# Optimization experiments

Hardware: AMD Instinct MI355X
Metric: run time of the kernel (lower is better)

## Reference

```python
import jax, jax.numpy as jnp
import numpy as np

B, D, NH = 32768, 32, 128
SCALE = 0.05  # weight init scale; keeps exp(s) well-conditioned


def setup_inputs() -> dict:
    key = jax.random.key(0)
    ks = jax.random.split(key, 10)
    x = jax.random.normal(ks[0], (B, D), jnp.float32)
    # layer 0: LeafParam(2) -> learned constant (s, t)
    p0 = jax.random.normal(ks[1], (2,), jnp.float32) * SCALE
    # per-dim MLPs for i = 1..D-1, stacked. Layer i consumes x[:, :i]; we pad
    # its first weight to (D, NH) with rows >= i zeroed so a single batched
    # einsum computes all per-dim nets at once (same math as the python loop).
    mask = (jnp.arange(D)[None, :] < jnp.arange(1, D)[:, None]).astype(jnp.float32)  # (D-1, D)
    W1 = jax.random.normal(ks[2], (D - 1, D, NH), jnp.float32) * SCALE * mask[:, :, None]
    b1 = jax.random.normal(ks[3], (D - 1, NH), jnp.float32) * SCALE
    W2 = jax.random.normal(ks[4], (D - 1, NH, NH), jnp.float32) * SCALE
    b2 = jax.random.normal(ks[5], (D - 1, NH), jnp.float32) * SCALE
    W3 = jax.random.normal(ks[6], (D - 1, NH, NH), jnp.float32) * SCALE
    b3 = jax.random.normal(ks[7], (D - 1, NH), jnp.float32) * SCALE
    W4 = jax.random.normal(ks[8], (D - 1, NH, 2), jnp.float32) * SCALE
    b4 = jax.random.normal(ks[9], (D - 1, 2), jnp.float32) * SCALE
    return dict(x=x, p0=p0, W1=W1, b1=b1, W2=W2, b2=b2, W3=W3, b3=b3, W4=W4, b4=b4)


def _lrelu(h):
    return jnp.where(h >= 0, h, 0.2 * h)  # LeakyReLU(0.2)


def reference(x, p0, W1, b1, W2, b2, W3, b3, W4, b4):
    # All D-1 per-dim MLPs in parallel. W1 rows >= i are zero, so
    h = _lrelu(jnp.einsum('bd,idh->bih', x, W1) + b1[None])     # (B, D-1, NH)
    h = _lrelu(jnp.einsum('bih,ihk->bik', h, W2) + b2[None])
    h = _lrelu(jnp.einsum('bih,ihk->bik', h, W3) + b3[None])
    st = jnp.einsum('bih,iho->bio', h, W4) + b4[None]           # (B, D-1, 2)
    st0 = jnp.broadcast_to(p0[None, None, :], (x.shape[0], 1, 2))
    st = jnp.concatenate([st0, st], axis=1)                     # (B, D, 2)
    s, t = st[..., 0], st[..., 1]
    z = x * jnp.exp(s) + t      # parity=True -> order is the identity permutation
    log_det = jnp.sum(s, axis=1)                                # (B,)
    return z, log_det
```

## Files before the change

kernel.cpp:

```cpp
#include <hip/hip_runtime.h>

typedef __bf16 v8bf  __attribute__((ext_vector_type(8)));
typedef float  f32x4  __attribute__((ext_vector_type(4)));
typedef float  f32x16 __attribute__((ext_vector_type(16)));
typedef unsigned int u32;
typedef u32 u32x4 __attribute__((ext_vector_type(4)));
typedef unsigned short u16;

#define NI   31
#define DD   32
#define NHID 128
#define NROW 32768
#define NCHUNK 64
#define ITERS  2
#define NET_EL 36864
#define W2F_EL 4096
#define W3F_EL 20480
#define LDS_W4T 73728
#define LDS_BB  74240
#define LDS_BYTES 75008

__device__ __forceinline__ u32 cvtpk(float lo, float hi) {
    u32 r;
    asm("v_cvt_pk_bf16_f32 %0, %1, %2" : "=v"(r) : "v"(lo), "v"(hi));
    return r;
}

__device__ __forceinline__ void repack_tile(const f32x16 c, v8bf* f0, v8bf* f1) {
    f32x16 v;
    #pragma unroll
    for (int r = 0; r < 16; ++r) { float x = c[r]; v[r] = fmaxf(x, 0.2f * x); }
    #pragma unroll
    for (int p = 0; p < 2; ++p) {
        u32 a0 = cvtpk(v[8*p + 0], v[8*p + 1]);
        u32 a1 = cvtpk(v[8*p + 2], v[8*p + 3]);
        u32 b0 = cvtpk(v[8*p + 4], v[8*p + 5]);
        u32 b1 = cvtpk(v[8*p + 6], v[8*p + 7]);
        asm("v_permlane32_swap_b32 %0, %1" : "+v"(a0), "+v"(b0));
        asm("v_permlane32_swap_b32 %0, %1" : "+v"(a1), "+v"(b1));
        u32x4 wd = {a0, a1, b0, b1};
        if (p == 0) *f0 = __builtin_bit_cast(v8bf, wd);
        else        *f1 = __builtin_bit_cast(v8bf, wd);
    }
}

__global__ void maf_prep(const float* __restrict__ W1, const float* __restrict__ W2,
                         const float* __restrict__ W3, __bf16* __restrict__ blob,
                         __bf16* __restrict__ xfrag, const float* __restrict__ x) {
    int b = blockIdx.x, t = threadIdx.x;
    if (b < 3 * NI) {
        __shared__ float panel[16 * 128];
        int kind = b / NI, i = b % NI;
        const float* src; __bf16* dst; int NKS;
        if (kind == 0)      { src = W2 + (size_t)i * NHID * NHID; dst = blob + (size_t)i * NET_EL + W2F_EL; NKS = 8; }
        else if (kind == 1) { src = W3 + (size_t)i * NHID * NHID; dst = blob + (size_t)i * NET_EL + W3F_EL; NKS = 8; }
        else                { src = W1 + (size_t)i * DD * NHID;   dst = blob + (size_t)i * NET_EL;          NKS = 2; }
        const int fo = t & 127, hi2 = t >> 7;
        const int mt = fo >> 5, c = fo & 31;
        for (int ksb = 0; ksb < NKS; ++ksb) {
            #pragma unroll
            for (int r = 0; r < 8; ++r) {
                int e = r * 256 + t;
                panel[e] = src[(size_t)(ksb * 16 + (e >> 7)) * NHID + (e & 127)];
            }
            __syncthreads();
            __bf16 tmp[8];
            #pragma unroll
            for (int j = 0; j < 8; ++j) tmp[j] = (__bf16)panel[(hi2 * 8 + j) * 128 + fo];
            *(u32x4*)&dst[((size_t)(mt * NKS + ksb) * 64 + hi2 * 32 + c) * 8] = *(u32x4*)tmp;
            __syncthreads();
        }
    } else {
        __shared__ float pan[64 * 33];
        const int xb = b - 3 * NI;
        for (int pass = 0; pass < 4; ++pass) {
            const int rb = xb * 256 + pass * 64;
            #pragma unroll
            for (int r = 0; r < 8; ++r) {
                int e = r * 256 + t;
                pan[(e >> 5) * 33 + (e & 31)] = x[(size_t)(rb + (e >> 5)) * DD + (e & 31)];
            }
            __syncthreads();
            {
                int w2 = t >> 6, l = t & 63;
                int nt = w2 >> 1, ks = w2 & 1;
                int c = l & 31, hi = l >> 5;
                const float* pr = &pan[(nt * 32 + c) * 33 + ks * 16 + hi * 8];
                f32x4 x0 = *(const f32x4*)pr;
                f32x4 x1 = *(const f32x4*)(pr + 4);
                u32x4 wd = {cvtpk(x0[0], x0[1]), cvtpk(x0[2], x0[3]),
                            cvtpk(x1[0], x1[1]), cvtpk(x1[2], x1[3])};
                *(u32x4*)&xfrag[(size_t)(rb >> 6) * 2048 + ((w2 * 64 + l) << 3)] = wd;
            }
            __syncthreads();
        }
    }
}

__global__ __launch_bounds__(256, 2) void maf_main(
    const __bf16* __restrict__ xfrag, const __bf16* __restrict__ blob,
    const float* __restrict__ b1, const float* __restrict__ b2,
    const float* __restrict__ b3,
    const float* __restrict__ W4, const float* __restrict__ b4,
    float* __restrict__ sT, __bf16* __restrict__ tT) {

    extern __shared__ __align__(16) char smem[];
    __bf16* w4t = (__bf16*)(smem + LDS_W4T);
    __bf16* bb  = (__bf16*)(smem + LDS_BB);
    const __bf16* wlds = (const __bf16*)smem;

    const int t = threadIdx.x;
    const int i = blockIdx.x / NCHUNK;
    const int chunk = blockIdx.x % NCHUNK;
    const int l = t & 63, w = t >> 6, c = l & 31, hi = l >> 5;
    const bool full_k1 = (i >= 16);

    f32x16 acc[4][2];
    v8bf Bf[2][8];
    v8bf Bx[2][2];

#define LOADX(G)                                                                      \
    { const __bf16* xg = xfrag + (size_t)(G) * 2048;                                  \
      Bx[0][0] = *(const v8bf*)&xg[(0 * 64 + l) << 3];                                \
      if (full_k1) Bx[0][1] = *(const v8bf*)&xg[(1 * 64 + l) << 3];                   \
      Bx[1][0] = *(const v8bf*)&xg[(2 * 64 + l) << 3];                                \
      if (full_k1) Bx[1][1] = *(const v8bf*)&xg[(3 * 64 + l) << 3]; }

    LOADX((chunk * (ITERS * 256) + w * 64) >> 6)

    {
        const u32x4* src = (const u32x4*)(blob + (size_t)i * NET_EL);
        u32x4* dst = (u32x4*)smem;
        #pragma unroll
        for (int k = 0; k < 18; ++k) dst[k * 256 + t] = src[k * 256 + t];
        w4t[t] = (__bf16)W4[(size_t)i * 2 * NHID + (t & 127) * 2 + (t >> 7)];
        if (t < NHID) {
            bb[t]       = (__bf16)b1[i * NHID + t];
            bb[128 + t] = (__bf16)b2[i * NHID + t];
            bb[256 + t] = (__bf16)b3[i * NHID + t];
        }
    }
    __syncthreads();

    const u32 ones0 = (hi == 0) ? 0x3F80u : 0u;
    const v8bf Bones = __builtin_bit_cast(v8bf, (u32x4){ones0, 0u, 0u, 0u});
    const float s0 = b4[2 * i], t0 = b4[2 * i + 1];
    const f32x16 zz = {};

#define ABIAS(BOFF, MT)                                                               \
    __builtin_bit_cast(v8bf, (u32x4){                                                 \
        (hi == 0) ? (u32)__builtin_bit_cast(u16, bb[(BOFF) + (MT) * 32 + c]) : 0u,    \
        0u, 0u, 0u})

#define HIDDEN(BASE_EL, BOFF)                                                         \
    {                                                                                 \
        _Pragma("unroll")                                                             \
        for (int mt = 0; mt < 4; ++mt) {                                              \
            v8bf Ab = ABIAS(BOFF, mt);                                                \
            acc[mt][0] = __builtin_amdgcn_mfma_f32_32x32x16_bf16(Ab, Bones, zz, 0, 0, 0); \
            acc[mt][1] = __builtin_amdgcn_mfma_f32_32x32x16_bf16(Ab, Bones, zz, 0, 0, 0); \
        }                                                                             \
        _Pragma("unroll")                                                             \
        for (int ks = 0; ks < 8; ++ks) {                                              \
            v8bf A[4];                                                                \
            _Pragma("unroll")                                                         \
            for (int mt = 0; mt < 4; ++mt)                                            \
                A[mt] = *(const v8bf*)&wlds[(BASE_EL) + ((mt * 8 + ks) * 64 + l) * 8]; \
            _Pragma("unroll")                                                         \
            for (int mt = 0; mt < 4; ++mt)                                            \
                _Pragma("unroll")                                                     \
                for (int nt = 0; nt < 2; ++nt)                                        \
                    acc[mt][nt] = __builtin_amdgcn_mfma_f32_32x32x16_bf16(            \
                        A[mt], Bf[nt][ks], acc[mt][nt], 0, 0, 0);                     \
        }                                                                             \
        _Pragma("unroll")                                                             \
        for (int mt = 0; mt < 4; ++mt)                                                \
            _Pragma("unroll")                                                         \
            for (int nt = 0; nt < 2; ++nt)                                            \
                repack_tile(acc[mt][nt], &Bf[nt][2 * mt], &Bf[nt][2 * mt + 1]);       \
    }

    #pragma unroll 1
    for (int it = 0; it < ITERS; ++it) {
        const int row0 = chunk * (ITERS * 256) + it * 256 + w * 64;

        #pragma unroll
        for (int mt = 0; mt < 4; ++mt) {
            v8bf Ab = ABIAS(0, mt);
            v8bf A0 = *(const v8bf*)&wlds[((mt * 2 + 0) * 64 + l) * 8];
            v8bf A1;
            if (full_k1) A1 = *(const v8bf*)&wlds[((mt * 2 + 1) * 64 + l) * 8];
            #pragma unroll
            for (int nt = 0; nt < 2; ++nt) {
                f32x16 a = __builtin_amdgcn_mfma_f32_32x32x16_bf16(Ab, Bones, zz, 0, 0, 0);
                a = __builtin_amdgcn_mfma_f32_32x32x16_bf16(A0, Bx[nt][0], a, 0, 0, 0);
                if (full_k1)
                    a = __builtin_amdgcn_mfma_f32_32x32x16_bf16(A1, Bx[nt][1], a, 0, 0, 0);
                acc[mt][nt] = a;
            }
        }
        #pragma unroll
        for (int mt = 0; mt < 4; ++mt)
            #pragma unroll
            for (int nt = 0; nt < 2; ++nt)
                repack_tile(acc[mt][nt], &Bf[nt][2 * mt], &Bf[nt][2 * mt + 1]);

        if (it + 1 < ITERS)
            LOADX((chunk * (ITERS * 256) + (it + 1) * 256 + w * 64) >> 6)

        HIDDEN(W2F_EL, 128)
        HIDDEN(W3F_EL, 256)

        {
            f32x16 acc4[2];
            acc4[0] = zz; acc4[1] = zz;
            #pragma unroll
            for (int ks = 0; ks < 8; ++ks) {
                v8bf a4 = {};
                if (c < 2) a4 = *(const v8bf*)&w4t[c * NHID + ks * 16 + hi * 8];
                acc4[0] = __builtin_amdgcn_mfma_f32_32x32x16_bf16(a4, Bf[0][ks], acc4[0], 0, 0, 0);
                acc4[1] = __builtin_amdgcn_mfma_f32_32x32x16_bf16(a4, Bf[1][ks], acc4[1], 0, 0, 0);
            }
            if (hi == 0) {
                #pragma unroll
                for (int nt = 0; nt < 2; ++nt) {
                    int row = row0 + nt * 32 + c;
                    sT[(size_t)i * NROW + row] = acc4[nt][0] + s0;
                    tT[(size_t)i * NROW + row] = (__bf16)(acc4[nt][1] + t0);
                }
            }
        }
    }
#undef LOADX
#undef ABIAS
#undef HIDDEN
}

__global__ void maf_fin(const float* __restrict__ x, const float* __restrict__ p0,
                        const float* __restrict__ sT, const __bf16* __restrict__ tT,
                        float* __restrict__ zout, float* __restrict__ ldout) {
    __shared__ float zsm[4 * 64 * 33];
    const int t = threadIdx.x, w = t >> 6, l = t & 63;
    const int rowbase = blockIdx.x * 256 + w * 64;
    const int row = rowbase + l;
    float* zs = zsm + w * (64 * 33);

    float xr[DD];
    #pragma unroll
    for (int q = 0; q < 8; ++q)
        *(f32x4*)&xr[q * 4] = *(const f32x4*)&x[(size_t)row * DD + q * 4];

    const float s0 = p0[0], t0 = p0[1];
    float ld = s0;
    zs[l * 33] = xr[0] * expf(s0) + t0;
    #pragma unroll
    for (int i = 0; i < NI; ++i) {
        float s  = sT[(size_t)i * NROW + row];
        float tt = (float)tT[(size_t)i * NROW + row];
        ld += s;
        zs[l * 33 + i + 1] = xr[i + 1] * expf(s) + tt;
    }
    ldout[row] = ld;
    #pragma unroll
    for (int j = 0; j < 32; ++j) {
        int f = j * 64 + l;
        zout[(size_t)rowbase * DD + f] = zs[(f >> 5) * 33 + (f & 31)];
    }
}

extern "C" void kernel_launch(void* const* d_in, const int* in_sizes, int n_in,
                              void* d_out, int out_size, void* d_ws, size_t ws_size,
                              hipStream_t stream) {
    (void)in_sizes; (void)n_in; (void)out_size; (void)ws_size;
    const float* x  = (const float*)d_in[0];
    const float* p0 = (const float*)d_in[1];
    const float* W1 = (const float*)d_in[2];
    const float* b1 = (const float*)d_in[3];
    const float* W2 = (const float*)d_in[4];
    const float* b2 = (const float*)d_in[5];
    const float* W3 = (const float*)d_in[6];
    const float* b3 = (const float*)d_in[7];
    const float* W4 = (const float*)d_in[8];
    const float* b4 = (const float*)d_in[9];

    float* zout  = (float*)d_out;
    float* ldout = zout + (size_t)NROW * DD;

    __bf16* blob  = (__bf16*)d_ws;
    __bf16* xfrag = blob + (size_t)NI * NET_EL;
    float*  sT    = (float*)(xfrag + (size_t)NROW * DD);
    __bf16* tT    = (__bf16*)(sT + (size_t)NI * NROW);

    hipFuncSetAttribute((const void*)maf_main,
                        hipFuncAttributeMaxDynamicSharedMemorySize, LDS_BYTES);

    maf_prep<<<3 * NI + 128, 256, 0, stream>>>(W1, W2, W3, blob, xfrag, x);
    maf_main<<<NI * NCHUNK, 256, LDS_BYTES, stream>>>(xfrag, blob, b1, b2, b3, W4, b4, sT, tT);
    maf_fin<<<NROW / 256, 256, 0, stream>>>(x, p0, sT, tT, zout, ldout);
}
```

Measured before the change: 102.2 us.

## Fold layer-1 bias into W1 via constant-one input column and trim bias MFMAs

The layer-1 bias is folded into an unused masked row of W1 (row 15 or 31), and the matching x column is set to 1 in two prepacked x fragment layouts. This removes the separate bias MFMAs in layer 1. In the hidden layers, only one bias MFMA per m-tile is issued and shared between both n-tiles at ks=0, instead of two. s_setprio hints are added around the MFMA bursts. The cost is an extra x fragment buffer written by the prep kernel and slightly more complex indexing, and the approach depends on the masked-zero rows of W1.

```diff
diff --git a/kernel.cpp b/kernel.cpp
--- a/kernel.cpp
+++ b/kernel.cpp
@@ -18,7 +18,7 @@
 #define W3F_EL 20480
 #define LDS_W4T 73728
 #define LDS_BB  74240
-#define LDS_BYTES 75008
+#define LDS_BYTES 74752
 
 __device__ __forceinline__ u32 cvtpk(float lo, float hi) {
     u32 r;
@@ -45,8 +45,10 @@
 }
 
 __global__ void maf_prep(const float* __restrict__ W1, const float* __restrict__ W2,
-                         const float* __restrict__ W3, __bf16* __restrict__ blob,
-                         __bf16* __restrict__ xfrag, const float* __restrict__ x) {
+                         const float* __restrict__ W3, const float* __restrict__ b1,
+                         __bf16* __restrict__ blob,
+                         __bf16* __restrict__ xfragB, __bf16* __restrict__ xfragA,
+                         const float* __restrict__ x) {
     int b = blockIdx.x, t = threadIdx.x;
     if (b < 3 * NI) {
         __shared__ float panel[16 * 128];
@@ -55,13 +57,17 @@
         if (kind == 0)      { src = W2 + (size_t)i * NHID * NHID; dst = blob + (size_t)i * NET_EL + W2F_EL; NKS = 8; }
         else if (kind == 1) { src = W3 + (size_t)i * NHID * NHID; dst = blob + (size_t)i * NET_EL + W3F_EL; NKS = 8; }
         else                { src = W1 + (size_t)i * DD * NHID;   dst = blob + (size_t)i * NET_EL;          NKS = 2; }
+        const int biasrow = (kind == 2) ? ((i <= 14) ? 15 : 31) : -1;
         const int fo = t & 127, hi2 = t >> 7;
         const int mt = fo >> 5, c = fo & 31;
         for (int ksb = 0; ksb < NKS; ++ksb) {
             #pragma unroll
             for (int r = 0; r < 8; ++r) {
                 int e = r * 256 + t;
-                panel[e] = src[(size_t)(ksb * 16 + (e >> 7)) * NHID + (e & 127)];
+                int grow = ksb * 16 + (e >> 7), gcol = e & 127;
+                float pv = src[(size_t)grow * NHID + gcol];
+                if (grow == biasrow) pv = b1[i * NHID + gcol];
+                panel[e] = pv;
             }
             __syncthreads();
             __bf16 tmp[8];
@@ -85,12 +91,22 @@
                 int w2 = t >> 6, l = t & 63;
                 int nt = w2 >> 1, ks = w2 & 1;
                 int c = l & 31, hi = l >> 5;
-                const float* pr = &pan[(nt * 32 + c) * 33 + ks * 16 + hi * 8];
-                f32x4 x0 = *(const f32x4*)pr;
-                f32x4 x1 = *(const f32x4*)(pr + 4);
-                u32x4 wd = {cvtpk(x0[0], x0[1]), cvtpk(x0[2], x0[3]),
-                            cvtpk(x1[0], x1[1]), cvtpk(x1[2], x1[3])};
-                *(u32x4*)&xfrag[(size_t)(rb >> 6) * 2048 + ((w2 * 64 + l) << 3)] = wd;
+                float vb[8], va[8];
+                #pragma unroll
+                for (int j = 0; j < 8; ++j) {
+                    int d = ks * 16 + hi * 8 + j;
+                    float pv = pan[(nt * 32 + c) * 33 + d];
+                    vb[j] = (d == 31) ? 1.0f : pv;
+                    va[j] = (d == 15) ? 1.0f : pv;
+                }
+                u32x4 wb_ = {cvtpk(vb[0], vb[1]), cvtpk(vb[2], vb[3]),
+                             cvtpk(vb[4], vb[5]), cvtpk(vb[6], vb[7])};
+                *(u32x4*)&xfragB[(size_t)(rb >> 6) * 2048 + ((w2 * 64 + l) << 3)] = wb_;
+                if (ks == 0) {
+                    u32x4 wa_ = {cvtpk(va[0], va[1]), cvtpk(va[2], va[3]),
+                                 cvtpk(va[4], va[5]), cvtpk(va[6], va[7])};
+                    *(u32x4*)&xfragA[(size_t)(rb >> 6) * 1024 + ((nt * 64 + l) << 3)] = wa_;
+                }
             }
             __syncthreads();
         }
@@ -98,9 +114,9 @@
 }
 
 __global__ __launch_bounds__(256, 2) void maf_main(
-    const __bf16* __restrict__ xfrag, const __bf16* __restrict__ blob,
-    const float* __restrict__ b1, const float* __restrict__ b2,
-    const float* __restrict__ b3,
+    const __bf16* __restrict__ xfragB, const __bf16* __restrict__ xfragA,
+    const __bf16* __restrict__ blob,
+    const float* __restrict__ b2, const float* __restrict__ b3,
     const float* __restrict__ W4, const float* __restrict__ b4,
     float* __restrict__ sT, __bf16* __restrict__ tT) {
 
@@ -113,18 +129,24 @@
     const int i = blockIdx.x / NCHUNK;
     const int chunk = blockIdx.x % NCHUNK;
     const int l = t & 63, w = t >> 6, c = l & 31, hi = l >> 5;
-    const bool full_k1 = (i >= 16);
+    const bool use_k1 = (i >= 15);
 
     f32x16 acc[4][2];
     v8bf Bf[2][8];
     v8bf Bx[2][2];
 
 #define LOADX(G)                                                                      \
-    { const __bf16* xg = xfrag + (size_t)(G) * 2048;                                  \
-      Bx[0][0] = *(const v8bf*)&xg[(0 * 64 + l) << 3];                                \
-      if (full_k1) Bx[0][1] = *(const v8bf*)&xg[(1 * 64 + l) << 3];                   \
-      Bx[1][0] = *(const v8bf*)&xg[(2 * 64 + l) << 3];                                \
-      if (full_k1) Bx[1][1] = *(const v8bf*)&xg[(3 * 64 + l) << 3]; }
+    { if (use_k1) {                                                                   \
+          const __bf16* xg = xfragB + (size_t)(G) * 2048;                             \
+          Bx[0][0] = *(const v8bf*)&xg[(0 * 64 + l) << 3];                            \
+          Bx[0][1] = *(const v8bf*)&xg[(1 * 64 + l) << 3];                            \
+          Bx[1][0] = *(const v8bf*)&xg[(2 * 64 + l) << 3];                            \
+          Bx[1][1] = *(const v8bf*)&xg[(3 * 64 + l) << 3];                            \
+      } else {                                                                        \
+          const __bf16* xg = xfragA + (size_t)(G) * 1024;                             \
+          Bx[0][0] = *(const v8bf*)&xg[(0 * 64 + l) << 3];                            \
+          Bx[1][0] = *(const v8bf*)&xg[(1 * 64 + l) << 3];                            \
+      } }
 
     LOADX((chunk * (ITERS * 256) + w * 64) >> 6)
 
@@ -135,9 +157,8 @@
         for (int k = 0; k < 18; ++k) dst[k * 256 + t] = src[k * 256 + t];
         w4t[t] = (__bf16)W4[(size_t)i * 2 * NHID + (t & 127) * 2 + (t >> 7)];
         if (t < NHID) {
-            bb[t]       = (__bf16)b1[i * NHID + t];
-            bb[128 + t] = (__bf16)b2[i * NHID + t];
-            bb[256 + t] = (__bf16)b3[i * NHID + t];
+            bb[t]       = (__bf16)b2[i * NHID + t];
+            bb[128 + t] = (__bf16)b3[i * NHID + t];
         }
     }
     __syncthreads();
@@ -147,32 +168,47 @@
     const float s0 = b4[2 * i], t0 = b4[2 * i + 1];
     const f32x16 zz = {};
 
-#define ABIAS(BOFF, MT)                                                               \
-    __builtin_bit_cast(v8bf, (u32x4){                                                 \
-        (hi == 0) ? (u32)__builtin_bit_cast(u16, bb[(BOFF) + (MT) * 32 + c]) : 0u,    \
-        0u, 0u, 0u})
-
-#define HIDDEN(BASE_EL, BOFF)                                                         \
+    u32 Abw[2][4];
+    #pragma unroll
+    for (int L = 0; L < 2; ++L)
+        #pragma unroll
+        for (int mt = 0; mt < 4; ++mt)
+            Abw[L][mt] = (hi == 0)
+                ? (u32)__builtin_bit_cast(u16, bb[L * NHID + mt * 32 + c]) : 0u;
+
+#define ABFRAG(L, MT) __builtin_bit_cast(v8bf, (u32x4){Abw[L][MT], 0u, 0u, 0u})
+
+#define HIDDEN(BASE_EL, L)                                                            \
     {                                                                                 \
         _Pragma("unroll")                                                             \
-        for (int mt = 0; mt < 4; ++mt) {                                              \
-            v8bf Ab = ABIAS(BOFF, mt);                                                \
-            acc[mt][0] = __builtin_amdgcn_mfma_f32_32x32x16_bf16(Ab, Bones, zz, 0, 0, 0); \
-            acc[mt][1] = __builtin_amdgcn_mfma_f32_32x32x16_bf16(Ab, Bones, zz, 0, 0, 0); \
-        }                                                                             \
+        for (int mt = 0; mt < 4; ++mt)                                                \
+            acc[mt][0] = __builtin_amdgcn_mfma_f32_32x32x16_bf16(                     \
+                ABFRAG(L, mt), Bones, zz, 0, 0, 0);                                   \
+        __builtin_amdgcn_s_setprio(1);                                                \
         _Pragma("unroll")                                                             \
         for (int ks = 0; ks < 8; ++ks) {                                              \
             v8bf A[4];                                                                \
             _Pragma("unroll")                                                         \
             for (int mt = 0; mt < 4; ++mt)                                            \
                 A[mt] = *(const v8bf*)&wlds[(BASE_EL) + ((mt * 8 + ks) * 64 + l) * 8]; \
-            _Pragma("unroll")                                                         \
-            for (int mt = 0; mt < 4; ++mt)                                            \
+            if (ks == 0) {                                                            \
                 _Pragma("unroll")                                                     \
-                for (int nt = 0; nt < 2; ++nt)                                        \
-                    acc[mt][nt] = __builtin_amdgcn_mfma_f32_32x32x16_bf16(            \
-                        A[mt], Bf[nt][ks], acc[mt][nt], 0, 0, 0);                     \
+                for (int mt = 0; mt < 4; ++mt) {                                      \
+                    acc[mt][1] = __builtin_amdgcn_mfma_f32_32x32x16_bf16(             \
+                        A[mt], Bf[1][0], acc[mt][0], 0, 0, 0);                        \
+                    acc[mt][0] = __builtin_amdgcn_mfma_f32_32x32x16_bf16(             \
+                        A[mt], Bf[0][0], acc[mt][0], 0, 0, 0);                        \
+                }                                                                     \
+            } else {                                                                  \
+                _Pragma("unroll")                                                     \
+                for (int mt = 0; mt < 4; ++mt)                                        \
+                    _Pragma("unroll")                                                 \
+                    for (int nt = 0; nt < 2; ++nt)                                    \
+                        acc[mt][nt] = __builtin_amdgcn_mfma_f32_32x32x16_bf16(        \
+                            A[mt], Bf[nt][ks], acc[mt][nt], 0, 0, 0);                 \
+            }                                                                         \
         }                                                                             \
+        __builtin_amdgcn_s_setprio(0);                                                \
         _Pragma("unroll")                                                             \
         for (int mt = 0; mt < 4; ++mt)                                                \
             _Pragma("unroll")                                                         \
@@ -184,21 +220,21 @@
     for (int it = 0; it < ITERS; ++it) {
         const int row0 = chunk * (ITERS * 256) + it * 256 + w * 64;
 
+        __builtin_amdgcn_s_setprio(1);
         #pragma unroll
         for (int mt = 0; mt < 4; ++mt) {
-            v8bf Ab = ABIAS(0, mt);
             v8bf A0 = *(const v8bf*)&wlds[((mt * 2 + 0) * 64 + l) * 8];
             v8bf A1;
-            if (full_k1) A1 = *(const v8bf*)&wlds[((mt * 2 + 1) * 64 + l) * 8];
+            if (use_k1) A1 = *(const v8bf*)&wlds[((mt * 2 + 1) * 64 + l) * 8];
             #pragma unroll
             for (int nt = 0; nt < 2; ++nt) {
-                f32x16 a = __builtin_amdgcn_mfma_f32_32x32x16_bf16(Ab, Bones, zz, 0, 0, 0);
-                a = __builtin_amdgcn_mfma_f32_32x32x16_bf16(A0, Bx[nt][0], a, 0, 0, 0);
-                if (full_k1)
+                f32x16 a = __builtin_amdgcn_mfma_f32_32x32x16_bf16(A0, Bx[nt][0], zz, 0, 0, 0);
+                if (use_k1)
                     a = __builtin_amdgcn_mfma_f32_32x32x16_bf16(A1, Bx[nt][1], a, 0, 0, 0);
                 acc[mt][nt] = a;
             }
         }
+        __builtin_amdgcn_s_setprio(0);
         #pragma unroll
         for (int mt = 0; mt < 4; ++mt)
             #pragma unroll
@@ -208,8 +244,8 @@
         if (it + 1 < ITERS)
             LOADX((chunk * (ITERS * 256) + (it + 1) * 256 + w * 64) >> 6)
 
-        HIDDEN(W2F_EL, 128)
-        HIDDEN(W3F_EL, 256)
+        HIDDEN(W2F_EL, 0)
+        HIDDEN(W3F_EL, 1)
 
         {
             f32x16 acc4[2];
@@ -232,7 +268,7 @@
         }
     }
 #undef LOADX
-#undef ABIAS
+#undef ABFRAG
 #undef HIDDEN
 }
 
@@ -286,15 +322,17 @@
     float* zout  = (float*)d_out;
     float* ldout = zout + (size_t)NROW * DD;
 
-    __bf16* blob  = (__bf16*)d_ws;
-    __bf16* xfrag = blob + (size_t)NI * NET_EL;
-    float*  sT    = (float*)(xfrag + (size_t)NROW * DD);
-    __bf16* tT    = (__bf16*)(sT + (size_t)NI * NROW);
+    __bf16* blob   = (__bf16*)d_ws;
+    __bf16* xfragB = blob + (size_t)NI * NET_EL;
+    __bf16* xfragA = xfragB + (size_t)NROW * DD;
+    float*  sT     = (float*)(xfragA + (size_t)NROW * 16);
+    __bf16* tT     = (__bf16*)(sT + (size_t)NI * NROW);
 
     hipFuncSetAttribute((const void*)maf_main,
                         hipFuncAttributeMaxDynamicSharedMemorySize, LDS_BYTES);
 
-    maf_prep<<<3 * NI + 128, 256, 0, stream>>>(W1, W2, W3, blob, xfrag, x);
-    maf_main<<<NI * NCHUNK, 256, LDS_BYTES, stream>>>(xfrag, blob, b1, b2, b3, W4, b4, sT, tT);
+    maf_prep<<<3 * NI + 128, 256, 0, stream>>>(W1, W2, W3, b1, blob, xfragB, xfragA, x);
+    maf_main<<<NI * NCHUNK, 256, LDS_BYTES, stream>>>(xfragB, xfragA, blob,
+                                                      b2, b3, W4, b4, sT, tT);
     maf_fin<<<NROW / 256, 256, 0, stream>>>(x, p0, sT, tT, zout, ldout);
 }
```

Measured after the change: 102.6 us. About the same (+0.4%).
